# Optimization experiments

Hardware: AMD Instinct MI355X
Metric: run time of the kernel (lower is better)

Reference implementation:

```python
import jax, jax.numpy as jnp
import numpy as np

H = 1024   # hidden_size
V = 1024   # output_size
B = 64     # batch
L = 512    # seq_len


def setup_inputs() -> dict:
    key = jax.random.key(0)
    ks = jax.random.split(key, 14)
    n = jax.random.normal
    s = jnp.float32(0.02)
    return {
        "encoder_output": n(ks[0], (L, B, H), jnp.float32),
        "hidden": n(ks[1], (B, H), jnp.float32),
        "decoder_output": n(ks[2], (B, H), jnp.float32),
        "Wa": n(ks[3], (H, 2 * H), jnp.float32) * s,
        "ba": n(ks[4], (H,), jnp.float32) * s,
        "v": n(ks[5], (H,), jnp.float32) * s,
        "W_ih": n(ks[6], (3 * H, 2 * H), jnp.float32) * s,
        "b_ih": n(ks[7], (3 * H,), jnp.float32) * s,
        "W_hh": n(ks[8], (3 * H, H), jnp.float32) * s,
        "b_hh": n(ks[9], (3 * H,), jnp.float32) * s,
        "Wo": n(ks[10], (H, 3 * H), jnp.float32) * s,
        "bo": n(ks[11], (H,), jnp.float32) * s,
        "Wf": n(ks[12], (V, H), jnp.float32) * s,
        "bf": n(ks[13], (V,), jnp.float32) * s,
    }


def reference(encoder_output, hidden, decoder_output, Wa, ba, v,
              W_ih, b_ih, W_hh, b_hh, Wo, bo, Wf, bf):
    Lx, Bx, Hx = encoder_output.shape
    # energy[b,l] = v . (Wa @ cat(hidden[b], enc[l,b]) + ba)
    # split Wa into hidden-part and encoder-part; fold v into each (linearity)
    Wa_h, Wa_e = Wa[:, :Hx], Wa[:, Hx:]
    vh = Wa_h.T @ v            # (H,)
    ve = Wa_e.T @ v            # (H,)
    vb = ba @ v                # scalar
    # encoder contribution to energies is constant across decode steps
    enc_score = jnp.einsum('lbh,h->bl', encoder_output, ve)  # (B, L)

    def gru_cell(x, h):
        # torch.nn.GRUCell math, gate order [r, z, n]
        gi = x @ W_ih.T + b_ih
        gh = h @ W_hh.T + b_hh
        i_r, i_z, i_n = jnp.split(gi, 3, axis=1)
        h_r, h_z, h_n = jnp.split(gh, 3, axis=1)
        r = jax.nn.sigmoid(i_r + h_r)
        z = jax.nn.sigmoid(i_z + h_z)
        n_g = jnp.tanh(i_n + r * h_n)
        return (1.0 - z) * n_g + z * h

    def step(carry, _):
        h, dec = carry
        energy = (h @ vh + vb)[:, None] + enc_score          # (B, L)
        a = jax.nn.softmax(energy, axis=1)                   # softmax over seq
        ctx = jnp.einsum('bl,lbh->bh', a, encoder_output)    # (B, H)
        h_new = gru_cell(jnp.concatenate([dec, ctx], axis=1), h)
        dec_new = jax.nn.softmax(
            jnp.concatenate([h_new, dec, ctx], axis=1) @ Wo.T + bo, axis=1)
        out = jax.nn.softmax(dec_new @ Wf.T + bf, axis=1)    # (B, V)
        return (h_new, dec_new), out

    _, outs = jax.lax.scan(step, (hidden, decoder_output), None, length=Lx)
    return outs  # (L, B, V)
```

## Files before the change

kernel.cpp:

```cpp
#include <hip/hip_runtime.h>
#include <hip/hip_bf16.h>


#define HH 1024
#define BB 64
#define LL 512
#define VV 1024

typedef short bf16x8 __attribute__((ext_vector_type(8)));
typedef float f32x4 __attribute__((ext_vector_type(4)));

__device__ __forceinline__ short f2bf(float x) {
  union { float f; unsigned u; } a; a.f = x;
  unsigned r = (a.u + 0x7FFF + ((a.u >> 16) & 1)) >> 16;
  return (short)r;
}

__device__ __forceinline__ float fsig(float x) {
  return 1.0f / (1.0f + __expf(-x));
}
__device__ __forceinline__ float ftanh(float x) {
  float ex = __expf(2.0f * x);
  return 1.0f - 2.0f / (ex + 1.0f);
}

__device__ __forceinline__ unsigned long long ld64c(const void* p) {
  return __hip_atomic_load((const unsigned long long*)p, __ATOMIC_RELAXED, __HIP_MEMORY_SCOPE_AGENT);
}
__device__ __forceinline__ unsigned ld32c(const void* p) {
  return __hip_atomic_load((const unsigned*)p, __ATOMIC_RELAXED, __HIP_MEMORY_SCOPE_AGENT);
}
__device__ __forceinline__ void st32c(void* p, unsigned v) {
  __hip_atomic_store((unsigned*)p, v, __ATOMIC_RELAXED, __HIP_MEMORY_SCOPE_AGENT);
}
__device__ __forceinline__ void stfc(float* p, float v) {
  union { float f; unsigned u; } a; a.f = v;
  st32c(p, a.u);
}

static constexpr size_t OFF_VE    = 0;
static constexpr size_t OFF_ES    = 4096;
static constexpr size_t OFF_A     = OFF_ES    + 131072;
static constexpr size_t OFF_CTX   = OFF_A     + 131072;
static constexpr size_t OFF_GICTX = OFF_CTX   + 262144;
static constexpr size_t OFF_OC    = OFF_GICTX + 786432;
static constexpr size_t OFF_FLAGS = OFF_OC    + 262144;
static constexpr size_t OFF_PSUMB = OFF_FLAGS + 32768;
static constexpr size_t OFF_PSUMO = OFF_PSUMB + 16384;
static constexpr size_t OFF_E2    = OFF_PSUMO + 16384;
static constexpr size_t OFF_HB0   = OFF_E2    + 131072;
static constexpr size_t OFF_HB1   = OFF_HB0   + 131072;
static constexpr size_t OFF_PACKW = OFF_HB1   + 131072;


__global__ void K_init(const float* __restrict__ hidden, const float* __restrict__ dec0,
                       short* __restrict__ hb, short* __restrict__ e2,
                       unsigned* __restrict__ flags) {
  int tid = blockIdx.x * 256 + threadIdx.x;
  if (tid < BB * HH) {
    hb[tid] = f2bf(hidden[tid]);
    e2[tid] = f2bf(dec0[tid]);
  }
  if (tid < 8192) flags[tid] = 0u;
}

__global__ void K_ve(const float* __restrict__ Wa, const float* __restrict__ v, float* __restrict__ ve) {
  int i = blockIdx.x * 64 + threadIdx.x;
  float acc = 0.f;
  for (int k = 0; k < HH; ++k) acc += Wa[(size_t)k * 2048 + 1024 + i] * v[k];
  ve[i] = acc;
}

__global__ void K_escore(const float* __restrict__ enc, const float* __restrict__ ve, float* __restrict__ es) {
  int bid = blockIdx.x;
  int lane = threadIdx.x;
  const float* row = enc + (size_t)bid * HH;
  float acc = 0.f;
  #pragma unroll
  for (int i = 0; i < 16; ++i) { int k = lane + 64 * i; acc += row[k] * ve[k]; }
  for (int m = 1; m < 64; m <<= 1) acc += __shfl_xor(acc, m);
  if (lane == 0) { int l = bid >> 6, b = bid & 63; es[b * LL + l] = acc; }
}

__global__ void K_asm(const float* __restrict__ es, float* __restrict__ a) {
  __shared__ float red[256];
  int b = blockIdx.x, tid = threadIdx.x;
  float e0 = es[b * LL + tid], e1 = es[b * LL + 256 + tid];
  red[tid] = fmaxf(e0, e1);
  __syncthreads();
  for (int s = 128; s > 0; s >>= 1) { if (tid < s) red[tid] = fmaxf(red[tid], red[tid + s]); __syncthreads(); }
  float M = red[0];
  __syncthreads();
  float x0 = expf(e0 - M), x1 = expf(e1 - M);
  red[tid] = x0 + x1;
  __syncthreads();
  for (int s = 128; s > 0; s >>= 1) { if (tid < s) red[tid] += red[tid + s]; __syncthreads(); }
  float S = red[0];
  a[b * LL + tid] = x0 / S;
  a[b * LL + 256 + tid] = x1 / S;
}

__global__ void K_ctx(const float* __restrict__ enc, const float* __restrict__ a, float* __restrict__ ctx) {
  int b = blockIdx.x >> 3, hc = blockIdx.x & 7;
  int h = hc * 128 + threadIdx.x;
  float acc = 0.f;
  for (int l = 0; l < LL; ++l) acc += a[b * LL + l] * enc[(size_t)(l * BB + b) * HH + h];
  ctx[b * HH + h] = acc;
}

__global__ void K_gictx(const float* __restrict__ ctx, const float* __restrict__ W_ih, const float* __restrict__ b_ih,
                        const float* __restrict__ Wo, const float* __restrict__ bo,
                        float* __restrict__ gictx, float* __restrict__ oc) {
  int c = blockIdx.x;
  int b = threadIdx.x;
  float acc = 0.f;
  if (c < 3072) {
    for (int k = 0; k < HH; ++k) acc += ctx[b * HH + k] * W_ih[(size_t)c * 2048 + 1024 + k];
    gictx[b * 3072 + c] = acc + b_ih[c];
  } else {
    int c2 = c - 3072;
    for (int k = 0; k < HH; ++k) acc += ctx[b * HH + k] * Wo[(size_t)c2 * 3072 + 2048 + k];
    oc[b * HH + c2] = acc + bo[c2];
  }
}

__global__ void K_pack(const float* __restrict__ W_ih, const float* __restrict__ W_hh,
                       const float* __restrict__ Wo, const float* __restrict__ Wf, short* __restrict__ packW) {
  int tid = blockIdx.x * 64 + threadIdx.x;
  int lane = tid & 63;
  int ks = (tid >> 6) & 31;
  int tile = (tid >> 11) % 9;
  int cg = tid / (9 * 32 * 64);
  int n = lane & 15;
  int k0 = ks * 32 + (lane >> 4) * 8;
  int row = cg * 16 + n;
  const float* src;
  size_t base;
  switch (tile) {
    case 0: base = (size_t)row * 2048;               src = W_ih; break;
    case 1: base = (size_t)(1024 + row) * 2048;      src = W_ih; break;
    case 2: base = (size_t)(2048 + row) * 2048;      src = W_ih; break;
    case 3: base = (size_t)row * 3072 + 1024;        src = Wo;   break;
    case 4: base = (size_t)row * 1024;               src = W_hh; break;
    case 5: base = (size_t)(1024 + row) * 1024;      src = W_hh; break;
    case 6: base = (size_t)(2048 + row) * 1024;      src = W_hh; break;
    case 7: base = (size_t)row * 1024;               src = Wf;   break;
    default: base = (size_t)row * 3072;              src = Wo;   break;
  }
  bf16x8 vv;
  #pragma unroll
  for (int j = 0; j < 8; ++j) vv[j] = f2bf(src[base + k0 + j]);
  ((bf16x8*)packW)[tid] = vv;
}


#define STAGE_SLICE(dst, srcbase)                                              \
  do {                                                                         \
    const int chunk_ = (wave + (cg & 3)) & 3;                                  \
    const short* pA_ = (srcbase) + (chunk_ << 12) + (lane << 3);               \
    const short* pB_ = pA_ + 2048;                                             \
    f32x4 t0_, t1_, t2_, t3_, t4_, t5_, t6_, t7_;                              \
    asm volatile(                                                              \
      "global_load_dwordx4 %0, %8, off sc0 sc1\n\t"                            \
      "global_load_dwordx4 %1, %8, off offset:1024 sc0 sc1\n\t"                \
      "global_load_dwordx4 %2, %8, off offset:2048 sc0 sc1\n\t"                \
      "global_load_dwordx4 %3, %8, off offset:3072 sc0 sc1\n\t"                \
      "global_load_dwordx4 %4, %9, off sc0 sc1\n\t"                            \
      "global_load_dwordx4 %5, %9, off offset:1024 sc0 sc1\n\t"                \
      "global_load_dwordx4 %6, %9, off offset:2048 sc0 sc1\n\t"                \
      "global_load_dwordx4 %7, %9, off offset:3072 sc0 sc1\n\t"                \
      "s_waitcnt vmcnt(0)"                                                     \
      : "=&v"(t0_), "=&v"(t1_), "=&v"(t2_), "=&v"(t3_),                        \
        "=&v"(t4_), "=&v"(t5_), "=&v"(t6_), "=&v"(t7_)                         \
      : "v"(pA_), "v"(pB_)                                                     \
      : "memory");                                                             \
    f32x4 tv_[8] = {t0_, t1_, t2_, t3_, t4_, t5_, t6_, t7_};                   \
    _Pragma("unroll")                                                          \
    for (int i_ = 0; i_ < 8; ++i_) {                                           \
      int off_ = (chunk_ << 12) + (i_ << 9) + (lane << 3);                     \
      int r_ = off_ >> 10;                                                     \
      int sw_ = ((off_ & 1023) << 1) ^ ((r_ & 7) << 4);                        \
      *(f32x4*)&(dst)[(r_ << 10) + (sw_ >> 1)] = tv_[i_];                      \
    }                                                                          \
    __builtin_amdgcn_sched_barrier(0);                                         \
  } while (0)

#define LFRAG(buf, ks) \
  (*(const bf16x8*)&(buf)[((llo) << 10) + (((((ks) * 64) + (lhi << 4)) ^ ((llo & 7) << 4)) >> 1)])

__global__ __launch_bounds__(256, 1) void K_step(
    const bf16x8* __restrict__ packW,
    short* __restrict__ e2, short* __restrict__ hb,
    const float* __restrict__ hidden,
    float* __restrict__ psumB, float* __restrict__ psumO,
    const float* __restrict__ gictx, const float* __restrict__ ocbuf,
    const float* __restrict__ b_hh, const float* __restrict__ bfv,
    float* __restrict__ outp, unsigned* __restrict__ flags) {
  const int wg = blockIdx.x;
  const int rg = wg & 3;
  const int cg = wg >> 2;
  const int tid = threadIdx.x;
  const int wave = tid >> 6;
  const int lane = tid & 63;
  const int lhi = lane >> 4;
  const int llo = lane & 15;

  __shared__ short se2[16 * 1024];
  __shared__ short sh[16 * 1024];
  __shared__ float lds_g[6][16][17];
  __shared__ float lds_p[5][16][17];
  __shared__ float lds_rs[16];

  const int wbase = cg * (9 * 32 * 64) + lane;
  const int t0 = wave * 2, t1 = wave * 2 + 1;

  bf16x8 wA0[32], wA1[32], wB8[8];
  #pragma unroll
  for (int ks = 0; ks < 32; ++ks) {
    wA0[ks] = packW[wbase + (t0 * 32 + ks) * 64];
    wA1[ks] = packW[wbase + (t1 * 32 + ks) * 64];
  }
  #pragma unroll
  for (int i = 0; i < 8; ++i) wB8[i] = packW[wbase + (8 * 32 + wave * 8 + i) * 64];
  #pragma unroll
  for (int ks = 0; ks < 32; ++ks) {
    asm volatile("" : "+v"(wA0[ks]));
    asm volatile("" : "+v"(wA1[ks]));
  }
  #pragma unroll
  for (int i = 0; i < 8; ++i) asm volatile("" : "+v"(wB8[i]));

  const int row = tid >> 4, col = tid & 15;
  const int b_ = rg * 16 + row, j = cg * 16 + col;
  const float c_gr  = gictx[b_ * 3072 + j]        + b_hh[j];
  const float c_gz  = gictx[b_ * 3072 + 1024 + j] + b_hh[1024 + j];
  const float c_gn  = gictx[b_ * 3072 + 2048 + j];
  const float c_ghn = b_hh[2048 + j];
  const float c_oc  = ocbuf[b_ * HH + j];
  float h_reg = hidden[b_ * HH + j];
  const float c_bf  = bfv[cg * 16 + llo];

  unsigned* myflags = flags + rg * (64 * 32);
  const short* e2slice = e2 + rg * 16384;
  short*       hslice  = hb + rg * 16384;

  STAGE_SLICE(sh, hslice);

  for (int t = 0; t <= LL; ++t) {
    unsigned long long pc[8];
    if (wave == 0 && t >= 1) {
      const float* pp = psumB + rg * 1024 + llo * 64 + lhi * 16;
      #pragma unroll
      for (int i = 0; i < 8; ++i) pc[i] = ld64c(pp + i * 2);
    }
    STAGE_SLICE(se2, e2slice);
    __syncthreads();

    if (wave == 0) {
      float total = 1.0f;
      if (t >= 1) {
        float s = 0.f;
        #pragma unroll
        for (int i = 0; i < 8; ++i) {
          union { unsigned long long u; float f[2]; } c; c.u = pc[i];
          s += c.f[0] + c.f[1];
        }
        s += __shfl_xor(s, 16);
        s += __shfl_xor(s, 32);
        total = s;
      }
      if (lane < 16) lds_rs[lane] = 1.0f / total;
    }

    const short* A0 = (wave < 2) ? se2 : sh;
    f32x4 acc0 = {0.f, 0.f, 0.f, 0.f}, acc1 = {0.f, 0.f, 0.f, 0.f};
    #pragma unroll
    for (int ks = 0; ks < 32; ++ks) {
      bf16x8 af0 = LFRAG(A0, ks);
      bf16x8 af1 = (wave == 3) ? LFRAG(se2, ks) : af0;
      acc0 = __builtin_amdgcn_mfma_f32_16x16x32_bf16(af0, wA0[ks], acc0, 0, 0, 0);
      acc1 = __builtin_amdgcn_mfma_f32_16x16x32_bf16(af1, wA1[ks], acc1, 0, 0, 0);
    }

    f32x4 savedA2;
    if (wave == 0) {
      #pragma unroll
      for (int r = 0; r < 4; ++r) { lds_g[0][lhi*4+r][llo] = acc0[r]; lds_g[1][lhi*4+r][llo] = acc1[r]; }
    } else if (wave == 1) {
      #pragma unroll
      for (int r = 0; r < 4; ++r) { lds_g[2][lhi*4+r][llo] = acc0[r]; savedA2[r] = acc1[r]; }
    } else if (wave == 2) {
      #pragma unroll
      for (int r = 0; r < 4; ++r) { lds_g[3][lhi*4+r][llo] = acc0[r]; lds_g[4][lhi*4+r][llo] = acc1[r]; }
    } else {
      #pragma unroll
      for (int r = 0; r < 4; ++r) lds_g[5][lhi*4+r][llo] = acc0[r];
    }
    __syncthreads();

    f32x4 eo = {0.f, 0.f, 0.f, 0.f};
    if (wave == 3 && t >= 1) {
      #pragma unroll
      for (int r = 0; r < 4; ++r) eo[r] = __expf(acc1[r] * lds_rs[lhi*4+r] + c_bf);
      #pragma unroll
      for (int r = 0; r < 4; ++r) {
        float v_ = eo[r];
        v_ += __shfl_xor(v_, 1, 16); v_ += __shfl_xor(v_, 2, 16);
        v_ += __shfl_xor(v_, 4, 16); v_ += __shfl_xor(v_, 8, 16);
        if (llo == 0) stfc(psumO + rg * 1024 + (lhi*4+r) * 64 + cg, v_);
      }
    }

    {
      float rsr = lds_rs[row];
      float gr  = lds_g[0][row][col] * rsr + lds_g[3][row][col] + c_gr;
      float gz  = lds_g[1][row][col] * rsr + lds_g[4][row][col] + c_gz;
      float gin = lds_g[2][row][col] * rsr + c_gn;
      float ghn = lds_g[5][row][col] + c_ghn;
      float rr = fsig(gr);
      float zz = fsig(gz);
      float nn = ftanh(gin + rr * ghn);
      float hnew = (1.0f - zz) * nn + zz * h_reg;
      h_reg = hnew;
      unsigned short hv = (unsigned short)f2bf(hnew);
      int other = __shfl_xor((int)hv, 1);
      if ((col & 1) == 0) {
        unsigned pk = (unsigned)hv | ((unsigned)(unsigned short)other << 16);
        st32c(hb + b_ * HH + (j & ~1), pk);
      }
    }

    {
      unsigned ep = 2u * (unsigned)t + 1u;
      __syncthreads();
      if (tid == 0) st32c(myflags + cg * 32, ep);
      if (wave == 0) {
        unsigned f;
        for (;;) {
          f = ld32c(myflags + lane * 32);
          if (!__any(f < ep)) break;
          __builtin_amdgcn_s_sleep(1);
        }
      }
      __syncthreads();
    }

    if (t < LL) {
      STAGE_SLICE(sh, hslice);
      __syncthreads();
      f32x4 accB = {0.f, 0.f, 0.f, 0.f};
      #pragma unroll
      for (int i = 0; i < 8; ++i) {
        int ks = wave * 8 + i;
        bf16x8 af = LFRAG(sh, ks);
        accB = __builtin_amdgcn_mfma_f32_16x16x32_bf16(af, wB8[i], accB, 0, 0, 0);
      }
      #pragma unroll
      for (int r = 0; r < 4; ++r) lds_p[wave][lhi*4+r][llo] = accB[r];
      if (wave == 1) {
        #pragma unroll
        for (int r = 0; r < 4; ++r) lds_p[4][lhi*4+r][llo] = savedA2[r];
      }
      __syncthreads();
      {
        float rsr = lds_rs[row];
        float l2 = lds_p[0][row][col] + lds_p[1][row][col] + lds_p[2][row][col] + lds_p[3][row][col]
                 + lds_p[4][row][col] * rsr + c_oc;
        float ev = __expf(l2);
        unsigned short eb = (unsigned short)f2bf(ev);
        int other = __shfl_xor((int)eb, 1);
        if ((col & 1) == 0) {
          unsigned pk = (unsigned)eb | ((unsigned)(unsigned short)other << 16);
          st32c(e2 + b_ * HH + (j & ~1), pk);
        }
        float sv = ev;
        sv += __shfl_xor(sv, 1, 16); sv += __shfl_xor(sv, 2, 16);
        sv += __shfl_xor(sv, 4, 16); sv += __shfl_xor(sv, 8, 16);
        if (col == 0) stfc(psumB + rg * 1024 + row * 64 + cg, sv);
      }

      {
        unsigned ep = 2u * (unsigned)t + 2u;
        __syncthreads();
        if (tid == 0) st32c(myflags + cg * 32, ep);
        if (t >= 1 && wave == 3) {
          #pragma unroll
          for (int r = 0; r < 4; ++r) {
            int prow = lhi * 4 + r;
            const float* pp = psumO + rg * 1024 + prow * 64 + llo * 4;
            union { unsigned long long u; float f[2]; } c0, c1;
            c0.u = ld64c(pp); c1.u = ld64c(pp + 2);
            float s = c0.f[0] + c0.f[1] + c1.f[0] + c1.f[1];
            s += __shfl_xor(s, 1, 16); s += __shfl_xor(s, 2, 16);
            s += __shfl_xor(s, 4, 16); s += __shfl_xor(s, 8, 16);
            int b2 = rg * 16 + prow;
            outp[(size_t)(t - 1) * BB * VV + (size_t)b2 * VV + cg * 16 + llo] = eo[r] / s;
          }
        }
        if (wave == 0) {
          unsigned f;
          for (;;) {
            f = ld32c(myflags + lane * 32);
            if (!__any(f < ep)) break;
            __builtin_amdgcn_s_sleep(1);
          }
        }
        __syncthreads();
      }
    } else {
      if (wave == 3) {
        #pragma unroll
        for (int r = 0; r < 4; ++r) {
          int prow = lhi * 4 + r;
          const float* pp = psumO + rg * 1024 + prow * 64 + llo * 4;
          union { unsigned long long u; float f[2]; } c0, c1;
          c0.u = ld64c(pp); c1.u = ld64c(pp + 2);
          float s = c0.f[0] + c0.f[1] + c1.f[0] + c1.f[1];
          s += __shfl_xor(s, 1, 16); s += __shfl_xor(s, 2, 16);
          s += __shfl_xor(s, 4, 16); s += __shfl_xor(s, 8, 16);
          int b2 = rg * 16 + prow;
          outp[(size_t)(t - 1) * BB * VV + (size_t)b2 * VV + cg * 16 + llo] = eo[r] / s;
        }
      }
    }
  }
}


extern "C" void kernel_launch(void* const* d_in, const int* in_sizes, int n_in,
                              void* d_out, int out_size, void* d_ws, size_t ws_size,
                              hipStream_t stream) {
  (void)in_sizes; (void)n_in; (void)out_size; (void)ws_size;
  const float* enc    = (const float*)d_in[0];
  const float* hidden = (const float*)d_in[1];
  const float* dec0   = (const float*)d_in[2];
  const float* Wa     = (const float*)d_in[3];
  const float* v      = (const float*)d_in[5];
  const float* W_ih   = (const float*)d_in[6];
  const float* b_ih   = (const float*)d_in[7];
  const float* W_hh   = (const float*)d_in[8];
  const float* b_hh   = (const float*)d_in[9];
  const float* Wo     = (const float*)d_in[10];
  const float* bo     = (const float*)d_in[11];
  const float* Wf     = (const float*)d_in[12];
  const float* bfv    = (const float*)d_in[13];

  char* ws = (char*)d_ws;
  float* ve    = (float*)(ws + OFF_VE);
  float* es    = (float*)(ws + OFF_ES);
  float* attn  = (float*)(ws + OFF_A);
  float* ctx   = (float*)(ws + OFF_CTX);
  float* gictx = (float*)(ws + OFF_GICTX);
  float* oc    = (float*)(ws + OFF_OC);
  unsigned* flags = (unsigned*)(ws + OFF_FLAGS);
  float* psumB = (float*)(ws + OFF_PSUMB);
  float* psumO = (float*)(ws + OFF_PSUMO);
  short* e2    = (short*)(ws + OFF_E2);
  short* hb    = (short*)(ws + OFF_HB0);
  short* packW = (short*)(ws + OFF_PACKW);

  hipLaunchKernelGGL(K_init, dim3(256), dim3(256), 0, stream, hidden, dec0, hb, e2, flags);
  hipLaunchKernelGGL(K_ve, dim3(16), dim3(64), 0, stream, Wa, v, ve);
  hipLaunchKernelGGL(K_escore, dim3(LL * BB), dim3(64), 0, stream, enc, ve, es);
  hipLaunchKernelGGL(K_asm, dim3(BB), dim3(256), 0, stream, es, attn);
  hipLaunchKernelGGL(K_ctx, dim3(512), dim3(128), 0, stream, enc, attn, ctx);
  hipLaunchKernelGGL(K_gictx, dim3(4096), dim3(64), 0, stream, ctx, W_ih, b_ih, Wo, bo, gictx, oc);
  hipLaunchKernelGGL(K_pack, dim3(64 * 9 * 32), dim3(64), 0, stream, W_ih, W_hh, Wo, Wf, packW);
  hipLaunchKernelGGL(K_step, dim3(256), dim3(256), 0, stream,
                     (const bf16x8*)packW, e2, hb, hidden, psumB, psumO,
                     gictx, oc, b_hh, bfv, (float*)d_out, flags);
}
```

Measured before the change: 5.038 ms.

## Merge two column groups per workgroup to halve persistent grid size

The persistent step kernel now runs 128 workgroups of 512 threads instead of 256 of 256. Each workgroup handles two 16-column groups, one per half of its waves. Both halves share a single staged copy of the e2/h slices in LDS, and each thread loads half as much in the staging macro. The per-step cross-workgroup flag barrier now polls 32 flags instead of 64, which cuts global synchronisation and duplicated LDS staging traffic. The cost is more register and LDS pressure per workgroup, and block-wide syncs now span eight waves.

```diff
diff --git a/kernel.cpp b/kernel.cpp
--- a/kernel.cpp
+++ b/kernel.cpp
@@ -156,28 +156,22 @@
 
 #define STAGE_SLICE(dst, srcbase)                                              \
   do {                                                                         \
-    const int chunk_ = (wave + (cg & 3)) & 3;                                  \
-    const short* pA_ = (srcbase) + (chunk_ << 12) + (lane << 3);               \
-    const short* pB_ = pA_ + 2048;                                             \
-    f32x4 t0_, t1_, t2_, t3_, t4_, t5_, t6_, t7_;                              \
+    const int chunk_ = (wave + cg) & 7;                                        \
+    const short* pA_ = (srcbase) + (chunk_ << 11) + (lane << 3);               \
+    f32x4 t0_, t1_, t2_, t3_;                                                  \
     asm volatile(                                                              \
-      "global_load_dwordx4 %0, %8, off sc0 sc1\n\t"                            \
-      "global_load_dwordx4 %1, %8, off offset:1024 sc0 sc1\n\t"                \
-      "global_load_dwordx4 %2, %8, off offset:2048 sc0 sc1\n\t"                \
-      "global_load_dwordx4 %3, %8, off offset:3072 sc0 sc1\n\t"                \
-      "global_load_dwordx4 %4, %9, off sc0 sc1\n\t"                            \
-      "global_load_dwordx4 %5, %9, off offset:1024 sc0 sc1\n\t"                \
-      "global_load_dwordx4 %6, %9, off offset:2048 sc0 sc1\n\t"                \
-      "global_load_dwordx4 %7, %9, off offset:3072 sc0 sc1\n\t"                \
+      "global_load_dwordx4 %0, %4, off sc0 sc1\n\t"                            \
+      "global_load_dwordx4 %1, %4, off offset:1024 sc0 sc1\n\t"                \
+      "global_load_dwordx4 %2, %4, off offset:2048 sc0 sc1\n\t"                \
+      "global_load_dwordx4 %3, %4, off offset:3072 sc0 sc1\n\t"                \
       "s_waitcnt vmcnt(0)"                                                     \
-      : "=&v"(t0_), "=&v"(t1_), "=&v"(t2_), "=&v"(t3_),                        \
-        "=&v"(t4_), "=&v"(t5_), "=&v"(t6_), "=&v"(t7_)                         \
-      : "v"(pA_), "v"(pB_)                                                     \
+      : "=&v"(t0_), "=&v"(t1_), "=&v"(t2_), "=&v"(t3_)                         \
+      : "v"(pA_)                                                               \
       : "memory");                                                             \
-    f32x4 tv_[8] = {t0_, t1_, t2_, t3_, t4_, t5_, t6_, t7_};                   \
+    f32x4 tv_[4] = {t0_, t1_, t2_, t3_};                                       \
     _Pragma("unroll")                                                          \
-    for (int i_ = 0; i_ < 8; ++i_) {                                           \
-      int off_ = (chunk_ << 12) + (i_ << 9) + (lane << 3);                     \
+    for (int i_ = 0; i_ < 4; ++i_) {                                           \
+      int off_ = (chunk_ << 11) + (i_ << 9) + (lane << 3);                     \
       int r_ = off_ >> 10;                                                     \
       int sw_ = ((off_ & 1023) << 1) ^ ((r_ & 7) << 4);                        \
       *(f32x4*)&(dst)[(r_ << 10) + (sw_ >> 1)] = tv_[i_];                      \
@@ -188,7 +182,7 @@
 #define LFRAG(buf, ks) \
   (*(const bf16x8*)&(buf)[((llo) << 10) + (((((ks) * 64) + (lhi << 4)) ^ ((llo & 7) << 4)) >> 1)])
 
-__global__ __launch_bounds__(256, 1) void K_step(
+__global__ __launch_bounds__(512, 1) void K_step(
     const bf16x8* __restrict__ packW,
     short* __restrict__ e2, short* __restrict__ hb,
     const float* __restrict__ hidden,
@@ -201,18 +195,21 @@
   const int cg = wg >> 2;
   const int tid = threadIdx.x;
   const int wave = tid >> 6;
+  const int w4 = wave & 3;
+  const int half = wave >> 2;
+  const int cg2 = cg * 2 + half;
   const int lane = tid & 63;
   const int lhi = lane >> 4;
   const int llo = lane & 15;
 
   __shared__ short se2[16 * 1024];
   __shared__ short sh[16 * 1024];
-  __shared__ float lds_g[6][16][17];
-  __shared__ float lds_p[5][16][17];
+  __shared__ float lds_g[2][6][16][17];
+  __shared__ float lds_p[2][5][16][17];
   __shared__ float lds_rs[16];
 
-  const int wbase = cg * (9 * 32 * 64) + lane;
-  const int t0 = wave * 2, t1 = wave * 2 + 1;
+  const int wbase = cg2 * (9 * 32 * 64) + lane;
+  const int t0 = w4 * 2, t1 = w4 * 2 + 1;
 
   bf16x8 wA0[32], wA1[32], wB8[8];
   #pragma unroll
@@ -221,7 +218,7 @@
     wA1[ks] = packW[wbase + (t1 * 32 + ks) * 64];
   }
   #pragma unroll
-  for (int i = 0; i < 8; ++i) wB8[i] = packW[wbase + (8 * 32 + wave * 8 + i) * 64];
+  for (int i = 0; i < 8; ++i) wB8[i] = packW[wbase + (8 * 32 + w4 * 8 + i) * 64];
   #pragma unroll
   for (int ks = 0; ks < 32; ++ks) {
     asm volatile("" : "+v"(wA0[ks]));
@@ -230,17 +227,17 @@
   #pragma unroll
   for (int i = 0; i < 8; ++i) asm volatile("" : "+v"(wB8[i]));
 
-  const int row = tid >> 4, col = tid & 15;
-  const int b_ = rg * 16 + row, j = cg * 16 + col;
+  const int row = (tid >> 4) & 15, col = tid & 15;
+  const int b_ = rg * 16 + row, j = cg2 * 16 + col;
   const float c_gr  = gictx[b_ * 3072 + j]        + b_hh[j];
   const float c_gz  = gictx[b_ * 3072 + 1024 + j] + b_hh[1024 + j];
   const float c_gn  = gictx[b_ * 3072 + 2048 + j];
   const float c_ghn = b_hh[2048 + j];
   const float c_oc  = ocbuf[b_ * HH + j];
   float h_reg = hidden[b_ * HH + j];
-  const float c_bf  = bfv[cg * 16 + llo];
-
-  unsigned* myflags = flags + rg * (64 * 32);
+  const float c_bf  = bfv[cg2 * 16 + llo];
+
+  unsigned* myflags = flags + rg * (32 * 32);
   const short* e2slice = e2 + rg * 16384;
   short*       hslice  = hb + rg * 16384;
 
@@ -272,34 +269,34 @@
       if (lane < 16) lds_rs[lane] = 1.0f / total;
     }
 
-    const short* A0 = (wave < 2) ? se2 : sh;
+    const short* A0 = (w4 < 2) ? se2 : sh;
     f32x4 acc0 = {0.f, 0.f, 0.f, 0.f}, acc1 = {0.f, 0.f, 0.f, 0.f};
     #pragma unroll
     for (int ks = 0; ks < 32; ++ks) {
       bf16x8 af0 = LFRAG(A0, ks);
-      bf16x8 af1 = (wave == 3) ? LFRAG(se2, ks) : af0;
+      bf16x8 af1 = (w4 == 3) ? LFRAG(se2, ks) : af0;
       acc0 = __builtin_amdgcn_mfma_f32_16x16x32_bf16(af0, wA0[ks], acc0, 0, 0, 0);
       acc1 = __builtin_amdgcn_mfma_f32_16x16x32_bf16(af1, wA1[ks], acc1, 0, 0, 0);
     }
 
     f32x4 savedA2;
-    if (wave == 0) {
-      #pragma unroll
-      for (int r = 0; r < 4; ++r) { lds_g[0][lhi*4+r][llo] = acc0[r]; lds_g[1][lhi*4+r][llo] = acc1[r]; }
-    } else if (wave == 1) {
-      #pragma unroll
-      for (int r = 0; r < 4; ++r) { lds_g[2][lhi*4+r][llo] = acc0[r]; savedA2[r] = acc1[r]; }
-    } else if (wave == 2) {
-      #pragma unroll
-      for (int r = 0; r < 4; ++r) { lds_g[3][lhi*4+r][llo] = acc0[r]; lds_g[4][lhi*4+r][llo] = acc1[r]; }
+    if (w4 == 0) {
+      #pragma unroll
+      for (int r = 0; r < 4; ++r) { lds_g[half][0][lhi*4+r][llo] = acc0[r]; lds_g[half][1][lhi*4+r][llo] = acc1[r]; }
+    } else if (w4 == 1) {
+      #pragma unroll
+      for (int r = 0; r < 4; ++r) { lds_g[half][2][lhi*4+r][llo] = acc0[r]; savedA2[r] = acc1[r]; }
+    } else if (w4 == 2) {
+      #pragma unroll
+      for (int r = 0; r < 4; ++r) { lds_g[half][3][lhi*4+r][llo] = acc0[r]; lds_g[half][4][lhi*4+r][llo] = acc1[r]; }
     } else {
       #pragma unroll
-      for (int r = 0; r < 4; ++r) lds_g[5][lhi*4+r][llo] = acc0[r];
+      for (int r = 0; r < 4; ++r) lds_g[half][5][lhi*4+r][llo] = acc0[r];
     }
     __syncthreads();
 
     f32x4 eo = {0.f, 0.f, 0.f, 0.f};
-    if (wave == 3 && t >= 1) {
+    if (w4 == 3 && t >= 1) {
       #pragma unroll
       for (int r = 0; r < 4; ++r) eo[r] = __expf(acc1[r] * lds_rs[lhi*4+r] + c_bf);
       #pragma unroll
@@ -307,16 +304,16 @@
         float v_ = eo[r];
         v_ += __shfl_xor(v_, 1, 16); v_ += __shfl_xor(v_, 2, 16);
         v_ += __shfl_xor(v_, 4, 16); v_ += __shfl_xor(v_, 8, 16);
-        if (llo == 0) stfc(psumO + rg * 1024 + (lhi*4+r) * 64 + cg, v_);
+        if (llo == 0) stfc(psumO + rg * 1024 + (lhi*4+r) * 64 + cg2, v_);
       }
     }
 
     {
       float rsr = lds_rs[row];
-      float gr  = lds_g[0][row][col] * rsr + lds_g[3][row][col] + c_gr;
-      float gz  = lds_g[1][row][col] * rsr + lds_g[4][row][col] + c_gz;
-      float gin = lds_g[2][row][col] * rsr + c_gn;
-      float ghn = lds_g[5][row][col] + c_ghn;
+      float gr  = lds_g[half][0][row][col] * rsr + lds_g[half][3][row][col] + c_gr;
+      float gz  = lds_g[half][1][row][col] * rsr + lds_g[half][4][row][col] + c_gz;
+      float gin = lds_g[half][2][row][col] * rsr + c_gn;
+      float ghn = lds_g[half][5][row][col] + c_ghn;
       float rr = fsig(gr);
       float zz = fsig(gz);
       float nn = ftanh(gin + rr * ghn);
@@ -337,7 +334,7 @@
       if (wave == 0) {
         unsigned f;
         for (;;) {
-          f = ld32c(myflags + lane * 32);
+          f = ld32c(myflags + (lane & 31) * 32);
           if (!__any(f < ep)) break;
           __builtin_amdgcn_s_sleep(1);
         }
@@ -351,21 +348,21 @@
       f32x4 accB = {0.f, 0.f, 0.f, 0.f};
       #pragma unroll
       for (int i = 0; i < 8; ++i) {
-        int ks = wave * 8 + i;
+        int ks = w4 * 8 + i;
         bf16x8 af = LFRAG(sh, ks);
         accB = __builtin_amdgcn_mfma_f32_16x16x32_bf16(af, wB8[i], accB, 0, 0, 0);
       }
       #pragma unroll
-      for (int r = 0; r < 4; ++r) lds_p[wave][lhi*4+r][llo] = accB[r];
-      if (wave == 1) {
+      for (int r = 0; r < 4; ++r) lds_p[half][w4][lhi*4+r][llo] = accB[r];
+      if (w4 == 1) {
         #pragma unroll
-        for (int r = 0; r < 4; ++r) lds_p[4][lhi*4+r][llo] = savedA2[r];
+        for (int r = 0; r < 4; ++r) lds_p[half][4][lhi*4+r][llo] = savedA2[r];
       }
       __syncthreads();
       {
         float rsr = lds_rs[row];
-        float l2 = lds_p[0][row][col] + lds_p[1][row][col] + lds_p[2][row][col] + lds_p[3][row][col]
-                 + lds_p[4][row][col] * rsr + c_oc;
+        float l2 = lds_p[half][0][row][col] + lds_p[half][1][row][col] + lds_p[half][2][row][col]
+                 + lds_p[half][3][row][col] + lds_p[half][4][row][col] * rsr + c_oc;
         float ev = __expf(l2);
         unsigned short eb = (unsigned short)f2bf(ev);
         int other = __shfl_xor((int)eb, 1);
@@ -376,14 +373,14 @@
         float sv = ev;
         sv += __shfl_xor(sv, 1, 16); sv += __shfl_xor(sv, 2, 16);
         sv += __shfl_xor(sv, 4, 16); sv += __shfl_xor(sv, 8, 16);
-        if (col == 0) stfc(psumB + rg * 1024 + row * 64 + cg, sv);
+        if (col == 0) stfc(psumB + rg * 1024 + row * 64 + cg2, sv);
       }
 
       {
         unsigned ep = 2u * (unsigned)t + 2u;
         __syncthreads();
         if (tid == 0) st32c(myflags + cg * 32, ep);
-        if (t >= 1 && wave == 3) {
+        if (t >= 1 && w4 == 3) {
           #pragma unroll
           for (int r = 0; r < 4; ++r) {
             int prow = lhi * 4 + r;
@@ -394,13 +391,13 @@
             s += __shfl_xor(s, 1, 16); s += __shfl_xor(s, 2, 16);
             s += __shfl_xor(s, 4, 16); s += __shfl_xor(s, 8, 16);
             int b2 = rg * 16 + prow;
-            outp[(size_t)(t - 1) * BB * VV + (size_t)b2 * VV + cg * 16 + llo] = eo[r] / s;
+            outp[(size_t)(t - 1) * BB * VV + (size_t)b2 * VV + cg2 * 16 + llo] = eo[r] / s;
           }
         }
         if (wave == 0) {
           unsigned f;
           for (;;) {
-            f = ld32c(myflags + lane * 32);
+            f = ld32c(myflags + (lane & 31) * 32);
             if (!__any(f < ep)) break;
             __builtin_amdgcn_s_sleep(1);
           }
@@ -408,7 +405,7 @@
         __syncthreads();
       }
     } else {
-      if (wave == 3) {
+      if (w4 == 3) {
         #pragma unroll
         for (int r = 0; r < 4; ++r) {
           int prow = lhi * 4 + r;
@@ -419,7 +416,7 @@
           s += __shfl_xor(s, 1, 16); s += __shfl_xor(s, 2, 16);
           s += __shfl_xor(s, 4, 16); s += __shfl_xor(s, 8, 16);
           int b2 = rg * 16 + prow;
-          outp[(size_t)(t - 1) * BB * VV + (size_t)b2 * VV + cg * 16 + llo] = eo[r] / s;
+          outp[(size_t)(t - 1) * BB * VV + (size_t)b2 * VV + cg2 * 16 + llo] = eo[r] / s;
         }
       }
     }
@@ -466,7 +463,7 @@
   hipLaunchKernelGGL(K_ctx, dim3(512), dim3(128), 0, stream, enc, attn, ctx);
   hipLaunchKernelGGL(K_gictx, dim3(4096), dim3(64), 0, stream, ctx, W_ih, b_ih, Wo, bo, gictx, oc);
   hipLaunchKernelGGL(K_pack, dim3(64 * 9 * 32), dim3(64), 0, stream, W_ih, W_hh, Wo, Wf, packW);
-  hipLaunchKernelGGL(K_step, dim3(256), dim3(256), 0, stream,
+  hipLaunchKernelGGL(K_step, dim3(128), dim3(512), 0, stream,
                      (const bf16x8*)packW, e2, hb, hidden, psumB, psumO,
                      gictx, oc, b_hh, bfv, (float*)d_out, flags);
 }
```

New measurement: 16.52 ms. +227.9%, slower.
